# Performance work log

Measured on AMD Instinct MI355X. Metric: run time of the kernel, lower is better.

The kernel has to match this reference:

```python
import jax, jax.numpy as jnp
import numpy as np

B, S, H, I, E, R = 2, 2048, 4096, 11008, 4, 8
SCALE = 16.0 / 8.0  # lora_alpha / rank


def _lora(x, A, Bm):
    # x:[N,in], A:[R,in], Bm:[out,R] -> [N,out]
    return (x @ A.T) @ Bm.T * SCALE


def _tmoe(x, router, A, Bm):
    # dense softmax routing over E experts, each a rank-R LoRA
    gates = jax.nn.softmax(x @ router.T, axis=-1)          # [N,E]
    a = jnp.einsum('nh,erh->ner', x, A)                    # [N,E,R]
    return jnp.einsum('ne,ner,eor->no', gates, a, Bm) * SCALE


def _delta(xf, mask, vA, vB, router, tA, tB):
    # image tokens -> V-Adapter LoRA, text tokens -> T-MoE (kd_mode=False)
    return jnp.where(mask[:, None], _lora(xf, vA, vB), _tmoe(xf, router, tA, tB))


def setup_inputs() -> dict:
    key = jax.random.key(0)
    ks = jax.random.split(key, 21)
    w = lambda k, shape: jax.random.normal(k, shape, dtype=jnp.float32) * 0.02
    return {
        'x': jax.random.normal(ks[0], (B, S, H), dtype=jnp.float32) * 0.5,
        'image_mask': jax.random.randint(ks[1], (B, S), 0, 2) == 1,
        'Wg': w(ks[2], (I, H)), 'Wu': w(ks[3], (I, H)), 'Wd': w(ks[4], (H, I)),
        'va_gate_A': w(ks[5], (R, H)), 'va_gate_B': w(ks[6], (I, R)),
        'va_up_A': w(ks[7], (R, H)), 'va_up_B': w(ks[8], (I, R)),
        'va_down_A': w(ks[9], (R, I)), 'va_down_B': w(ks[10], (H, R)),
        'router_gate': w(ks[11], (E, H)), 'tm_gate_A': w(ks[12], (E, R, H)), 'tm_gate_B': w(ks[13], (E, I, R)),
        'router_up': w(ks[14], (E, H)), 'tm_up_A': w(ks[15], (E, R, H)), 'tm_up_B': w(ks[16], (E, I, R)),
        'router_down': w(ks[17], (E, I)), 'tm_down_A': w(ks[18], (E, R, I)), 'tm_down_B': w(ks[19], (E, H, R)),
    }


def reference(x, image_mask, Wg, Wu, Wd,
              va_gate_A, va_gate_B, va_up_A, va_up_B, va_down_A, va_down_B,
              router_gate, tm_gate_A, tm_gate_B,
              router_up, tm_up_A, tm_up_B,
              router_down, tm_down_A, tm_down_B):
    Bb, Ss, Hh = x.shape
    xf = x.reshape(-1, Hh)                                  # [N,H]
    m = image_mask.reshape(-1)                              # [N]
    gate = xf @ Wg.T + _delta(xf, m, va_gate_A, va_gate_B, router_gate, tm_gate_A, tm_gate_B)
    up = xf @ Wu.T + _delta(xf, m, va_up_A, va_up_B, router_up, tm_up_A, tm_up_B)
    inter = jax.nn.silu(gate) * up                          # [N,I]
    out = inter @ Wd.T + _delta(inter, m, va_down_A, va_down_B, router_down, tm_down_A, tm_down_B)
    return out.reshape(Bb, Ss, Hh)
```

## Files before the change

### kernel.cpp

```cpp
#include <hip/hip_runtime.h>
#include <hip/hip_bf16.h>
#include <stdint.h>


#define H_DIM 4096
#define I_DIM 11008
#define N_TOK 4096
#define R_RANK 8
#define K1P 4224
#define K2P 11136

typedef __attribute__((ext_vector_type(8))) __bf16 bf16x8;
typedef __attribute__((ext_vector_type(4))) __bf16 bf16x4;
typedef __attribute__((ext_vector_type(4))) float  f32x4;

__device__ __forceinline__ void gload16(const void* g, const void* lds_wave_base) {
  auto gp = (const __attribute__((address_space(1))) void*)(uintptr_t)g;
  auto lp = (__attribute__((address_space(3))) void*)(uintptr_t)lds_wave_base;
  __builtin_amdgcn_global_load_lds(gp, lp, 16, 0, 0);
}

#define BAR()   asm volatile("s_barrier" ::: "memory")
#define LGKM0() do { asm volatile("s_waitcnt lgkmcnt(0)" ::: "memory"); \
                     __builtin_amdgcn_sched_barrier(0); } while (0)

__device__ __forceinline__ void detect_mask(const void* mask, int t, int* okI, int* okF) {
  const unsigned int* mi = (const unsigned int*)mask;
  int bad_i = 0, bad_f = 0;
  for (int idx = t; idx < 1024; idx += 256) {
    unsigned v = mi[idx];
    bad_i |= !(v == 0u || v == 1u);
    bad_f |= !(v == 0u || v == 0x3f800000u);
  }
  if (bad_i) *okI = 0;
  if (bad_f) *okF = 0;
}
__device__ __forceinline__ bool read_mask(const void* mask, int n, int okI, int okF) {
  if (okI) return ((const int*)mask)[n] != 0;
  if (okF) return ((const float*)mask)[n] != 0.0f;
  return ((const unsigned char*)mask)[n] != 0;
}

__global__ __launch_bounds__(256)
void prepAll(const float* __restrict__ Wg, const float* __restrict__ Wu,
             const float* __restrict__ vBg, const float* __restrict__ tmBg,
             const float* __restrict__ vBu, const float* __restrict__ tmBu,
             const float* __restrict__ vAg, const float* __restrict__ tmAg, const float* __restrict__ rg,
             const float* __restrict__ vAu, const float* __restrict__ tmAu, const float* __restrict__ ru,
             const float* __restrict__ vAd, const float* __restrict__ tmAd, const float* __restrict__ rd,
             __bf16* __restrict__ Wcat, __bf16* __restrict__ W88b, __bf16* __restrict__ W44b) {
  int b = blockIdx.x, t = threadIdx.x;
  if (b < I_DIM) {
    int i = b;
    int grp = i >> 7, within = i & 127;
    const float4* g4 = (const float4*)(Wg + (size_t)i * H_DIM);
    const float4* u4 = (const float4*)(Wu + (size_t)i * H_DIM);
    __bf16* og = Wcat + (size_t)(grp * 256 + within) * K1P;
    __bf16* ou = Wcat + (size_t)(grp * 256 + 128 + within) * K1P;
    for (int c = t; c < H_DIM / 4; c += 256) {
      float4 v = g4[c];
      bf16x4 bb = {(__bf16)v.x, (__bf16)v.y, (__bf16)v.z, (__bf16)v.w};
      *(bf16x4*)(og + c * 4) = bb;
      v = u4[c];
      bf16x4 b2 = {(__bf16)v.x, (__bf16)v.y, (__bf16)v.z, (__bf16)v.w};
      *(bf16x4*)(ou + c * 4) = b2;
    }
    if (t < 128) {
      float gv = 0.f, uv = 0.f;
      if (t < 8) gv = 2.f * vBg[i * R_RANK + t];
      else if (t < 40) { int e = (t - 8) >> 3, r = (t - 8) & 7;
        gv = 2.f * tmBg[((size_t)e * I_DIM + i) * R_RANK + r]; }
      if (t >= 40 && t < 48) uv = 2.f * vBu[i * R_RANK + (t - 40)];
      else if (t >= 48 && t < 80) { int e = (t - 48) >> 3, r = (t - 48) & 7;
        uv = 2.f * tmBu[((size_t)e * I_DIM + i) * R_RANK + r]; }
      og[H_DIM + t] = (__bf16)gv;
      ou[H_DIM + t] = (__bf16)uv;
    }
  } else if (b < I_DIM + 88) {
    int r = b - I_DIM;
    const float* src;
    if      (r <  8) src = vAg  + (size_t)r * H_DIM;
    else if (r < 40) src = tmAg + (size_t)(r - 8) * H_DIM;
    else if (r < 44) src = rg   + (size_t)(r - 40) * H_DIM;
    else if (r < 52) src = vAu  + (size_t)(r - 44) * H_DIM;
    else if (r < 84) src = tmAu + (size_t)(r - 52) * H_DIM;
    else             src = ru   + (size_t)(r - 84) * H_DIM;
    __bf16* dst = W88b + (size_t)r * H_DIM;
    for (int c = t; c < H_DIM / 4; c += 256) {
      float4 v = ((const float4*)src)[c];
      bf16x4 bb = {(__bf16)v.x, (__bf16)v.y, (__bf16)v.z, (__bf16)v.w};
      *(bf16x4*)(dst + c * 4) = bb;
    }
  } else {
    int r = b - I_DIM - 88;
    const float* src = (r < 8)  ? vAd  + (size_t)r * I_DIM
                     : (r < 40) ? tmAd + (size_t)(r - 8) * I_DIM
                                : rd   + (size_t)(r - 40) * I_DIM;
    __bf16* dst = W44b + (size_t)r * I_DIM;
    for (int c = t; c < I_DIM / 4; c += 256) {
      float4 v = ((const float4*)src)[c];
      bf16x4 bb = {(__bf16)v.x, (__bf16)v.y, (__bf16)v.z, (__bf16)v.w};
      *(bf16x4*)(dst + c * 4) = bb;
    }
  }
}

__global__ __launch_bounds__(256)
void prep_wd(const float* __restrict__ Wd, const float* __restrict__ vBd,
             const float* __restrict__ tmBd, __bf16* __restrict__ Wda) {
  int o = blockIdx.x, t = threadIdx.x;
  const float4* w4 = (const float4*)(Wd + (size_t)o * I_DIM);
  __bf16* orow = Wda + (size_t)o * K2P;
  for (int c = t; c < I_DIM / 4; c += 256) {
    float4 v = w4[c];
    bf16x4 b = {(__bf16)v.x, (__bf16)v.y, (__bf16)v.z, (__bf16)v.w};
    *(bf16x4*)(orow + c * 4) = b;
  }
  if (t < 128) {
    float v = 0.f;
    if (t < 8) v = 2.f * vBd[o * R_RANK + t];
    else if (t < 40) { int e = (t - 8) >> 3, r = (t - 8) & 7;
      v = 2.f * tmBd[((size_t)e * H_DIM + o) * R_RANK + r]; }
    orow[I_DIM + t] = (__bf16)v;
  }
}

__global__ __launch_bounds__(256)
void prep_x(const float* __restrict__ x, const void* __restrict__ mask,
            const __bf16* __restrict__ W88b, __bf16* __restrict__ Xaug) {
  __shared__ __align__(16) float sx[4][H_DIM];
  __shared__ float dots[4][88];
  __shared__ int okI, okF;
  int t = threadIdx.x, n0 = blockIdx.x * 4;
  if (t == 0) { okI = 1; okF = 1; }
  __syncthreads();
  detect_mask(mask, t, &okI, &okF);
  for (int tok = 0; tok < 4; ++tok) {
    const float4* xr = (const float4*)(x + (size_t)(n0 + tok) * H_DIM);
    __bf16* orow = Xaug + (size_t)(n0 + tok) * K1P;
    for (int c = t; c < H_DIM / 4; c += 256) {
      float4 v = xr[c];
      *(float4*)&sx[tok][c * 4] = v;
      bf16x4 b = {(__bf16)v.x, (__bf16)v.y, (__bf16)v.z, (__bf16)v.w};
      *(bf16x4*)(orow + c * 4) = b;
    }
  }
  __syncthreads();
  int wv = t >> 6, ln = t & 63;
  for (int gi = 0; gi < 6; ++gi) {
    int g = wv + gi * 4;
    if (g >= 22) break;
    int i0 = g * 4;
    const __bf16* base = W88b + (size_t)i0 * H_DIM;
    float acc[4][4];
#pragma unroll
    for (int ii = 0; ii < 4; ++ii)
#pragma unroll
      for (int tk = 0; tk < 4; ++tk) acc[ii][tk] = 0.f;
    for (int j = 0; j < H_DIM / 256; ++j) {
      int h = j * 256 + ln * 4;
      float4 v0 = *(const float4*)&sx[0][h];
      float4 v1 = *(const float4*)&sx[1][h];
      float4 v2 = *(const float4*)&sx[2][h];
      float4 v3 = *(const float4*)&sx[3][h];
#pragma unroll
      for (int ii = 0; ii < 4; ++ii) {
        bf16x4 wb = *(const bf16x4*)(base + (size_t)ii * H_DIM + h);
        float wx = (float)wb[0], wy = (float)wb[1], wz = (float)wb[2], ww = (float)wb[3];
        acc[ii][0] = fmaf(v0.x, wx, fmaf(v0.y, wy, fmaf(v0.z, wz, fmaf(v0.w, ww, acc[ii][0]))));
        acc[ii][1] = fmaf(v1.x, wx, fmaf(v1.y, wy, fmaf(v1.z, wz, fmaf(v1.w, ww, acc[ii][1]))));
        acc[ii][2] = fmaf(v2.x, wx, fmaf(v2.y, wy, fmaf(v2.z, wz, fmaf(v2.w, ww, acc[ii][2]))));
        acc[ii][3] = fmaf(v3.x, wx, fmaf(v3.y, wy, fmaf(v3.z, wz, fmaf(v3.w, ww, acc[ii][3]))));
      }
    }
#pragma unroll
    for (int ii = 0; ii < 4; ++ii) {
#pragma unroll
      for (int tk = 0; tk < 4; ++tk) {
        float a = acc[ii][tk];
        for (int s = 32; s > 0; s >>= 1) a += __shfl_xor(a, s);
        if (ln == 0) dots[tk][i0 + ii] = a;
      }
    }
  }
  __syncthreads();
  for (int pass = 0; pass < 2; ++pass) {
    int tok = (t >> 7) + pass * 2;
    int s = t & 127;
    const float* dd = dots[tok];
    bool img = read_mask(mask, n0 + tok, okI, okF);
    float c = 0.f;
    if (s < 80) {
      if (s < 40) {
        if (img) { if (s < 8) c = dd[s]; }
        else if (s >= 8) {
          float l0 = dd[40], l1 = dd[41], l2 = dd[42], l3 = dd[43];
          float mx = fmaxf(fmaxf(l0, l1), fmaxf(l2, l3));
          float e0 = __expf(l0 - mx), e1 = __expf(l1 - mx), e2 = __expf(l2 - mx), e3 = __expf(l3 - mx);
          float inv = 1.f / (e0 + e1 + e2 + e3);
          int e = (s - 8) >> 3;
          float ge = (e == 0 ? e0 : e == 1 ? e1 : e == 2 ? e2 : e3) * inv;
          c = ge * dd[s];
        }
      } else {
        int s2 = s - 40;
        if (img) { if (s2 < 8) c = dd[44 + s2]; }
        else if (s2 >= 8) {
          float l0 = dd[84], l1 = dd[85], l2 = dd[86], l3 = dd[87];
          float mx = fmaxf(fmaxf(l0, l1), fmaxf(l2, l3));
          float e0 = __expf(l0 - mx), e1 = __expf(l1 - mx), e2 = __expf(l2 - mx), e3 = __expf(l3 - mx);
          float inv = 1.f / (e0 + e1 + e2 + e3);
          int e = (s2 - 8) >> 3;
          float ge = (e == 0 ? e0 : e == 1 ? e1 : e == 2 ? e2 : e3) * inv;
          c = ge * dd[44 + s2];
        }
      }
    }
    Xaug[(size_t)(n0 + tok) * K1P + H_DIM + s] = (__bf16)c;
  }
}

__global__ __launch_bounds__(512)
void prep_x2(const void* __restrict__ mask, const __bf16* __restrict__ W44b,
             __bf16* __restrict__ X2) {
  __shared__ __align__(16) __bf16 si[2][I_DIM];
  __shared__ float dots[2][44];
  __shared__ int okI, okF;
  int t = threadIdx.x, n0 = blockIdx.x * 2;
  if (t == 0) { okI = 1; okF = 1; }
  __syncthreads();
  if (t < 256) detect_mask(mask, t, &okI, &okF);
  for (int tok = 0; tok < 2; ++tok) {
    const bf16x8* xr = (const bf16x8*)(X2 + (size_t)(n0 + tok) * K2P);
    bf16x8* srow = (bf16x8*)&si[tok][0];
    for (int c = t; c < I_DIM / 8; c += 512) srow[c] = xr[c];
  }
  __syncthreads();
  int wv = t >> 6, ln = t & 63;
  const bf16x8* s0 = (const bf16x8*)&si[0][0];
  const bf16x8* s1 = (const bf16x8*)&si[1][0];
  for (int gi = 0; gi < 2; ++gi) {
    int g = wv + gi * 8;
    if (g >= 11) break;
    int i0 = g * 4;
    const __bf16* base = W44b + (size_t)i0 * I_DIM;
    float acc[4][2];
#pragma unroll
    for (int ii = 0; ii < 4; ++ii) { acc[ii][0] = 0.f; acc[ii][1] = 0.f; }
    for (int j = 0; j < 22; ++j) {
      int ch = j * 64 + ln;
      if (ch < I_DIM / 8) {
        bf16x8 x0 = s0[ch], x1 = s1[ch];
        float xf0[8], xf1[8];
#pragma unroll
        for (int k = 0; k < 8; ++k) { xf0[k] = (float)x0[k]; xf1[k] = (float)x1[k]; }
#pragma unroll
        for (int ii = 0; ii < 4; ++ii) {
          bf16x8 wv8 = *(const bf16x8*)(base + (size_t)ii * I_DIM + ch * 8);
          float a0 = acc[ii][0], a1 = acc[ii][1];
#pragma unroll
          for (int k = 0; k < 8; ++k) {
            float wk = (float)wv8[k];
            a0 = fmaf(xf0[k], wk, a0);
            a1 = fmaf(xf1[k], wk, a1);
          }
          acc[ii][0] = a0; acc[ii][1] = a1;
        }
      }
    }
#pragma unroll
    for (int ii = 0; ii < 4; ++ii) {
#pragma unroll
      for (int tk = 0; tk < 2; ++tk) {
        float a = acc[ii][tk];
        for (int s = 32; s > 0; s >>= 1) a += __shfl_xor(a, s);
        if (ln == 0) dots[tk][i0 + ii] = a;
      }
    }
  }
  __syncthreads();
  if (t < 256) {
    int tok = t >> 7, s = t & 127;
    const float* dd = dots[tok];
    bool img = read_mask(mask, n0 + tok, okI, okF);
    float c = 0.f;
    if (s < 40) {
      if (img) { if (s < 8) c = dd[s]; }
      else if (s >= 8) {
        float l0 = dd[40], l1 = dd[41], l2 = dd[42], l3 = dd[43];
        float mx = fmaxf(fmaxf(l0, l1), fmaxf(l2, l3));
        float e0 = __expf(l0 - mx), e1 = __expf(l1 - mx), e2 = __expf(l2 - mx), e3 = __expf(l3 - mx);
        float inv = 1.f / (e0 + e1 + e2 + e3);
        int e = (s - 8) >> 3;
        float ge = (e == 0 ? e0 : e == 1 ? e1 : e == 2 ? e2 : e3) * inv;
        c = ge * dd[s];
      }
    }
    X2[(size_t)(n0 + tok) * K2P + I_DIM + s] = (__bf16)c;
  }
}

template<int MH, int NH>
__device__ __forceinline__ void mfmaq(f32x4 (&acc)[8][4], const bf16x8 (&av)[4][2],
                                      const bf16x8 (&bv)[2][2]) {
#pragma unroll
  for (int kk = 0; kk < 2; ++kk)
#pragma unroll
    for (int j = 0; j < 2; ++j)
#pragma unroll
      for (int i = 0; i < 4; ++i)
        acc[MH * 4 + i][NH * 2 + j] = __builtin_amdgcn_mfma_f32_16x16x32_bf16(
            av[i][kk], bv[j][kk], acc[MH * 4 + i][NH * 2 + j], 0, 0, 0);
}

template<int KS, int NT, int GN, typename OutT, int OSTR, int EPI, int MODE>
__global__ __launch_bounds__(512, 2)
void gemm256(const __bf16* __restrict__ A, const __bf16* __restrict__ Bm,
             OutT* __restrict__ C) {
  __shared__ __align__(16) char lds[131072];

  int t = threadIdx.x;
  int w = t >> 6, l = t & 63;
  int wm = w >> 2, wn = w & 3;
  int lrow = l & 15, kq = l >> 4;

  int nwg = gridDim.x, bid = blockIdx.x;
  int tm, tn;
  if constexpr (MODE == 1) {
    int x = bid & 7, i = bid >> 3;
    tm = ((x & 1) << 3) | (i & 7);
    tn = ((x >> 1) << 2) | (i >> 3);
  } else {
    int swz = (bid & 7) * (nwg >> 3) + (bid >> 3);
    tm = swz / GN; tn = swz % GN;
  }
  int m0 = tm * 256, n0 = tn * 256;

  int grow = (t >> 3) & 7;
  int gcole = ((t & 7) ^ grow) << 3;
  const __bf16* gA0 = A  + (size_t)(m0 + w * 8 + grow) * KS + gcole;
  const __bf16* gB0 = Bm + (size_t)(n0 + w * 8 + grow) * KS + gcole;
  char* ldsA0 = lds + w * 1024;
  char* ldsB0 = lds + 32768 + w * 1024;

  auto stageA = [&](int buf, int tt, int c) {
    gload16(gA0 + (size_t)c * (64 * KS) + (size_t)tt * 64,
            ldsA0 + buf * 65536 + c * 8192);
  };
  auto stageB = [&](int buf, int tt, int c) {
    gload16(gB0 + (size_t)c * (64 * KS) + (size_t)tt * 64,
            ldsB0 + buf * 65536 + c * 8192);
  };

  int aBase = (wm * 128 + lrow) * 128;
  int bBase = (wn * 64 + lrow) * 128;
  int sw    = (lrow & 7) << 4;
  int col0  = (kq * 16) ^ sw;
  int col1  = (64 + kq * 16) ^ sw;

  f32x4 acc[8][4];
#pragma unroll
  for (int i = 0; i < 8; ++i)
#pragma unroll
    for (int j = 0; j < 4; ++j) acc[i][j] = (f32x4){0.f, 0.f, 0.f, 0.f};

#pragma unroll
  for (int c = 0; c < 4; ++c) { stageA(0, 0, c); stageB(0, 0, c); }
#pragma unroll
  for (int c = 0; c < 4; ++c) { stageA(1, 1, c); stageB(1, 1, c); }
  asm volatile("s_waitcnt vmcnt(8)" ::: "memory");
  BAR();

  int cur = 0;
  for (int tt = 0; tt < NT; ++tt, cur ^= 1) {
    const char* sa = lds + (cur ? 65536 : 0);
    const char* sb = sa + 32768;
    int t2 = tt + 2;
    bool st = t2 < NT;
    bf16x8 aF[4][2], b0[2][2], b1[2][2];

#pragma unroll
    for (int i = 0; i < 4; ++i) {
      aF[i][0] = *(const bf16x8*)(sa + aBase + i * 2048 + col0);
      aF[i][1] = *(const bf16x8*)(sa + aBase + i * 2048 + col1);
    }
#pragma unroll
    for (int j = 0; j < 2; ++j) {
      b0[j][0] = *(const bf16x8*)(sb + bBase + j * 2048 + col0);
      b0[j][1] = *(const bf16x8*)(sb + bBase + j * 2048 + col1);
    }
    BAR(); LGKM0();
    __builtin_amdgcn_s_setprio(1);
    mfmaq<0, 0>(acc, aF, b0);
    __builtin_amdgcn_s_setprio(0);
    BAR();

    if (st) { stageA(cur, t2, 0); stageA(cur, t2, 2); }
#pragma unroll
    for (int j = 0; j < 2; ++j) {
      b1[j][0] = *(const bf16x8*)(sb + bBase + (2 + j) * 2048 + col0);
      b1[j][1] = *(const bf16x8*)(sb + bBase + (2 + j) * 2048 + col1);
    }
    BAR(); LGKM0();
    __builtin_amdgcn_s_setprio(1);
    mfmaq<0, 1>(acc, aF, b1);
    __builtin_amdgcn_s_setprio(0);
    BAR();

    if (st) { stageB(cur, t2, 0); stageB(cur, t2, 1); }
#pragma unroll
    for (int i = 0; i < 4; ++i) {
      aF[i][0] = *(const bf16x8*)(sa + aBase + (4 + i) * 2048 + col0);
      aF[i][1] = *(const bf16x8*)(sa + aBase + (4 + i) * 2048 + col1);
    }
    BAR(); LGKM0();
    __builtin_amdgcn_s_setprio(1);
    mfmaq<1, 0>(acc, aF, b0);
    __builtin_amdgcn_s_setprio(0);
    BAR();

    if (st) { stageB(cur, t2, 2); stageB(cur, t2, 3);
              stageA(cur, t2, 1); stageA(cur, t2, 3); }
    __builtin_amdgcn_s_setprio(1);
    mfmaq<1, 1>(acc, aF, b1);
    __builtin_amdgcn_s_setprio(0);
    if (st) asm volatile("s_waitcnt vmcnt(8)" ::: "memory");
    else    asm volatile("s_waitcnt vmcnt(0)" ::: "memory");
    BAR();
  }

  if constexpr (EPI == 0) {
    int r0 = m0 + wm * 128 + kq * 4;
    int c0 = n0 + wn * 64 + lrow;
#pragma unroll
    for (int mi = 0; mi < 8; ++mi) {
#pragma unroll
      for (int q = 0; q < 4; ++q) {
        OutT* p = C + (size_t)(r0 + mi * 16 + q) * OSTR + c0;
#pragma unroll
        for (int ni = 0; ni < 4; ++ni) p[ni * 16] = (OutT)acc[mi][ni][q];
      }
    }
  } else {
    float* xch = (float*)lds;
    bool isGate = (wn < 2);
    int p = wm * 2 + (wn & 1);
    float* mybuf = xch + (size_t)p * 8192 + (isGate ? 4096 : 0);
#pragma unroll
    for (int mi = 0; mi < 4; ++mi) {
      int msrc = isGate ? (4 + mi) : mi;
#pragma unroll
      for (int q = 0; q < 4; ++q) {
        int r = mi * 16 + kq * 4 + q;
        int key = (r >> 2) & 3;
#pragma unroll
        for (int ni = 0; ni < 4; ++ni) {
          int c = (ni * 16 + lrow) ^ (key << 4);
          mybuf[r * 64 + c] = acc[msrc][ni][q];
        }
      }
    }
    __syncthreads();
    const float* pbuf = xch + (size_t)p * 8192 + (isGate ? 0 : 4096);
    int mbase = isGate ? 0 : 4;
    int rowoff = isGate ? 0 : 64;
#pragma unroll
    for (int mi = 0; mi < 4; ++mi) {
#pragma unroll
      for (int q = 0; q < 4; ++q) {
        int r = mi * 16 + kq * 4 + q;
        int key = (r >> 2) & 3;
        int row = m0 + wm * 128 + rowoff + r;
        OutT* orow = C + (size_t)row * OSTR + tn * 128 + (wn & 1) * 64 + lrow;
#pragma unroll
        for (int ni = 0; ni < 4; ++ni) {
          int c = (ni * 16 + lrow) ^ (key << 4);
          float o = pbuf[r * 64 + c];
          float g = isGate ? acc[mbase + mi][ni][q] : o;
          float u = isGate ? o : acc[mbase + mi][ni][q];
          orow[ni * 16] = (OutT)(g / (1.f + __expf(-g)) * u);
        }
      }
    }
  }
}

extern "C" void kernel_launch(void* const* d_in, const int* in_sizes, int n_in,
                              void* d_out, int out_size, void* d_ws, size_t ws_size,
                              hipStream_t stream) {
  const float* x    = (const float*)d_in[0];
  const void*  mask = d_in[1];
  const float* Wg   = (const float*)d_in[2];
  const float* Wu   = (const float*)d_in[3];
  const float* Wd   = (const float*)d_in[4];
  const float* vAg  = (const float*)d_in[5];
  const float* vBg  = (const float*)d_in[6];
  const float* vAu  = (const float*)d_in[7];
  const float* vBu  = (const float*)d_in[8];
  const float* vAd  = (const float*)d_in[9];
  const float* vBd  = (const float*)d_in[10];
  const float* rg   = (const float*)d_in[11];
  const float* tmAg = (const float*)d_in[12];
  const float* tmBg = (const float*)d_in[13];
  const float* ru   = (const float*)d_in[14];
  const float* tmAu = (const float*)d_in[15];
  const float* tmBu = (const float*)d_in[16];
  const float* rd   = (const float*)d_in[17];
  const float* tmAd = (const float*)d_in[18];
  const float* tmBd = (const float*)d_in[19];

  char* ws = (char*)d_ws;
  __bf16* Xaug = (__bf16*)(ws);
  __bf16* Wcat = (__bf16*)(ws + 34603008);
  __bf16* X2   = (__bf16*)(ws + 220594176);
  __bf16* Wda  = (__bf16*)(ws + 311820288);
  __bf16* W88b = X2;
  __bf16* W44b = Wda;

  prepAll<<<I_DIM + 132, 256, 0, stream>>>(Wg, Wu, vBg, tmBg, vBu, tmBu,
                                           vAg, tmAg, rg, vAu, tmAu, ru,
                                           vAd, tmAd, rd, Wcat, W88b, W44b);
  prep_x<<<N_TOK / 4, 256, 0, stream>>>(x, mask, W88b, Xaug);

  gemm256<K1P, K1P / 64, 86, __bf16, K2P, 1, 0>
      <<<(N_TOK / 256) * 86, 512, 0, stream>>>(Xaug, Wcat, X2);

  prep_x2<<<N_TOK / 2, 512, 0, stream>>>(mask, W44b, X2);
  prep_wd<<<H_DIM, 256, 0, stream>>>(Wd, vBd, tmBd, Wda);

  gemm256<K2P, K2P / 64, H_DIM / 256, float, H_DIM, 0, 1>
      <<<(N_TOK / 256) * (H_DIM / 256), 512, 0, stream>>>(X2, Wda, (float*)d_out);
}
```

Baseline: 1.458 ms.

## Fuse Wd prep into prepAll, stage LoRA A weights in output, retile gemm1

```diff
diff --git a/kernel.cpp b/kernel.cpp
--- a/kernel.cpp
+++ b/kernel.cpp
@@ -43,12 +43,15 @@
 
 __global__ __launch_bounds__(256)
 void prepAll(const float* __restrict__ Wg, const float* __restrict__ Wu,
+             const float* __restrict__ Wd,
              const float* __restrict__ vBg, const float* __restrict__ tmBg,
              const float* __restrict__ vBu, const float* __restrict__ tmBu,
+             const float* __restrict__ vBd, const float* __restrict__ tmBd,
              const float* __restrict__ vAg, const float* __restrict__ tmAg, const float* __restrict__ rg,
              const float* __restrict__ vAu, const float* __restrict__ tmAu, const float* __restrict__ ru,
              const float* __restrict__ vAd, const float* __restrict__ tmAd, const float* __restrict__ rd,
-             __bf16* __restrict__ Wcat, __bf16* __restrict__ W88b, __bf16* __restrict__ W44b) {
+             __bf16* __restrict__ Wcat, __bf16* __restrict__ Wda,
+             __bf16* __restrict__ W88b, __bf16* __restrict__ W44b) {
   int b = blockIdx.x, t = threadIdx.x;
   if (b < I_DIM) {
     int i = b;
@@ -91,7 +94,7 @@
       bf16x4 bb = {(__bf16)v.x, (__bf16)v.y, (__bf16)v.z, (__bf16)v.w};
       *(bf16x4*)(dst + c * 4) = bb;
     }
-  } else {
+  } else if (b < I_DIM + 132) {
     int r = b - I_DIM - 88;
     const float* src = (r < 8)  ? vAd  + (size_t)r * I_DIM
                      : (r < 40) ? tmAd + (size_t)(r - 8) * I_DIM
@@ -102,26 +105,22 @@
       bf16x4 bb = {(__bf16)v.x, (__bf16)v.y, (__bf16)v.z, (__bf16)v.w};
       *(bf16x4*)(dst + c * 4) = bb;
     }
-  }
-}
-
-__global__ __launch_bounds__(256)
-void prep_wd(const float* __restrict__ Wd, const float* __restrict__ vBd,
-             const float* __restrict__ tmBd, __bf16* __restrict__ Wda) {
-  int o = blockIdx.x, t = threadIdx.x;
-  const float4* w4 = (const float4*)(Wd + (size_t)o * I_DIM);
-  __bf16* orow = Wda + (size_t)o * K2P;
-  for (int c = t; c < I_DIM / 4; c += 256) {
-    float4 v = w4[c];
-    bf16x4 b = {(__bf16)v.x, (__bf16)v.y, (__bf16)v.z, (__bf16)v.w};
-    *(bf16x4*)(orow + c * 4) = b;
-  }
-  if (t < 128) {
-    float v = 0.f;
-    if (t < 8) v = 2.f * vBd[o * R_RANK + t];
-    else if (t < 40) { int e = (t - 8) >> 3, r = (t - 8) & 7;
-      v = 2.f * tmBd[((size_t)e * H_DIM + o) * R_RANK + r]; }
-    orow[I_DIM + t] = (__bf16)v;
+  } else {
+    int o = b - I_DIM - 132;
+    const float4* w4 = (const float4*)(Wd + (size_t)o * I_DIM);
+    __bf16* orow = Wda + (size_t)o * K2P;
+    for (int c = t; c < I_DIM / 4; c += 256) {
+      float4 v = w4[c];
+      bf16x4 bb = {(__bf16)v.x, (__bf16)v.y, (__bf16)v.z, (__bf16)v.w};
+      *(bf16x4*)(orow + c * 4) = bb;
+    }
+    if (t < 128) {
+      float v = 0.f;
+      if (t < 8) v = 2.f * vBd[o * R_RANK + t];
+      else if (t < 40) { int e = (t - 8) >> 3, r = (t - 8) & 7;
+        v = 2.f * tmBd[((size_t)e * H_DIM + o) * R_RANK + r]; }
+      orow[I_DIM + t] = (__bf16)v;
+    }
   }
 }
 
@@ -327,9 +326,13 @@
   int nwg = gridDim.x, bid = blockIdx.x;
   int tm, tn;
   if constexpr (MODE == 1) {
-    int x = bid & 7, i = bid >> 3;
-    tm = ((x & 1) << 3) | (i & 7);
-    tn = ((x >> 1) << 2) | (i >> 3);
+    int xx = bid & 7, ii = bid >> 3;
+    tm = ((xx & 1) << 3) | (ii & 7);
+    tn = ((xx >> 1) << 2) | (ii >> 3);
+  } else if constexpr (MODE == 2) {
+    constexpr int FULL = (GN / 16) * 256;
+    if (bid < FULL) { int s = bid >> 8, ww = bid & 255; tm = ww & 15; tn = s * 16 + (ww >> 4); }
+    else            { int ww = bid - FULL; tm = ww & 15; tn = (GN / 16) * 16 + (ww >> 4); }
   } else {
     int swz = (bid & 7) * (nwg >> 3) + (bid >> 3);
     tm = swz / GN; tn = swz % GN;
@@ -514,19 +517,19 @@
   __bf16* Wcat = (__bf16*)(ws + 34603008);
   __bf16* X2   = (__bf16*)(ws + 220594176);
   __bf16* Wda  = (__bf16*)(ws + 311820288);
-  __bf16* W88b = X2;
-  __bf16* W44b = Wda;
-
-  prepAll<<<I_DIM + 132, 256, 0, stream>>>(Wg, Wu, vBg, tmBg, vBu, tmBu,
-                                           vAg, tmAg, rg, vAu, tmAu, ru,
-                                           vAd, tmAd, rd, Wcat, W88b, W44b);
+  __bf16* W88b = (__bf16*)d_out;
+  __bf16* W44b = (__bf16*)((char*)d_out + 1048576);
+
+  prepAll<<<I_DIM + 132 + H_DIM, 256, 0, stream>>>(
+      Wg, Wu, Wd, vBg, tmBg, vBu, tmBu, vBd, tmBd,
+      vAg, tmAg, rg, vAu, tmAu, ru, vAd, tmAd, rd,
+      Wcat, Wda, W88b, W44b);
   prep_x<<<N_TOK / 4, 256, 0, stream>>>(x, mask, W88b, Xaug);
 
-  gemm256<K1P, K1P / 64, 86, __bf16, K2P, 1, 0>
+  gemm256<K1P, K1P / 64, 86, __bf16, K2P, 1, 2>
       <<<(N_TOK / 256) * 86, 512, 0, stream>>>(Xaug, Wcat, X2);
 
   prep_x2<<<N_TOK / 2, 512, 0, stream>>>(mask, W44b, X2);
-  prep_wd<<<H_DIM, 256, 0, stream>>>(Wd, vBd, tmBd, Wda);
 
   gemm256<K2P, K2P / 64, H_DIM / 256, float, H_DIM, 0, 1>
       <<<(N_TOK / 256) * (H_DIM / 256), 512, 0, stream>>>(X2, Wda, (float*)d_out);
```

Result: no change. 1.445 ms (-0.9%).
